# Kernel optimization log

Hardware: AMD Instinct MI355X
Metric: run time of the kernel (lower is better)

Reference implementation:

```python
import jax, jax.numpy as jnp
import numpy as np

SHAPE_ = 32          # sqrt(max_seq_len); seq positions form a SHAPE_ x SHAPE_ grid
N_HEADS = 8
BATCH = 8
SEQ_LEN = SHAPE_ * SHAPE_  # 1024
HEAD_DIM = 64


def _construct_bias(w_, s):
    """bias[..., j, i] = w_rolled[..., s - i - 1 + j]  -> (1, h, s, s).
    'full' base type: roll last axis left by one (concat of w[...,1:] and w[...,0])."""
    w_ = jnp.concatenate([w_[..., 1:], w_[..., :1]], axis=-1)  # (1, h, 2s-1)
    j = jnp.arange(s)
    i = jnp.arange(s)
    idx = (s - 1 - i)[None, :] + j[:, None]  # (s_j, s_i), values in [0, 2s-2]
    return w_[..., idx]  # (1, h, s, s), axes (..., j, i)


def setup_inputs() -> dict:
    key = jax.random.key(0)
    k1, k2 = jax.random.split(key)
    v = jax.random.normal(k1, (BATCH, SEQ_LEN, N_HEADS, HEAD_DIM), dtype=jnp.float32)
    # learned 1D bias base, length 2*SHAPE_-1 for 'full' base type
    w = jax.random.normal(k2, (1, N_HEADS, 2 * SHAPE_ - 1), dtype=jnp.float32)
    return {"v": v, "w": w}


def reference(v, w):
    s = SHAPE_
    b, L, h, d = v.shape
    bias = _construct_bias(w, s)  # (1, h, s, s)
    # x_ = bias[:, :, None, :, None, :], y_ = bias[:, :, :, None, :, None]
    # w2[., h, a, b, c, e] = bias[., h, b, e] + bias[., h, a, c]  -> (1, h, s, s, s, s)
    w2 = bias[:, :, None, :, None, :] + bias[:, :, :, None, :, None]
    w2 = w2.reshape(1, h, s * s, s * s)  # (1, h, L, L)
    # original: repeat w2 over batch then einsum('nlhd,nhlj->njhd', v, transpose(w2, [0,1,3,2]))
    # => pbv[n, j, h, d] = sum_l v[n, l, h, d] * w2[0, h, j, l]; broadcast instead of repeat.
    return jnp.einsum('nlhd,hjl->njhd', v, w2[0])
```

## Files before the change

### kernel.cpp

```cpp
#include <hip/hip_runtime.h>
#include <hip/hip_bf16.h>


#define S 32
#define HD4 128

__global__ __launch_bounds__(128) void reduce_kernel(
    const float4* __restrict__ v, float4* __restrict__ Vc,
    float4* __restrict__ Ve) {
  int block = blockIdx.x;
  int t = threadIdx.x;
  bool isVc = block < 256;
  int b2 = isVc ? block : block - 256;
  int n = b2 >> 5;
  int x = b2 & 31;
  const float4* base = v + (size_t)n * 1024 * HD4 + t;
  float4 acc = make_float4(0.f, 0.f, 0.f, 0.f);
  if (isVc) {
#pragma unroll
    for (int c = 0; c < 32; ++c) {
      float4 r = base[(size_t)(c * S + x) * HD4];
      acc.x += r.x; acc.y += r.y; acc.z += r.z; acc.w += r.w;
    }
    Vc[(size_t)b2 * HD4 + t] = acc;
  } else {
#pragma unroll
    for (int e = 0; e < 32; ++e) {
      float4 r = base[(size_t)(x * S + e) * HD4];
      acc.x += r.x; acc.y += r.y; acc.z += r.z; acc.w += r.w;
    }
    Ve[(size_t)b2 * HD4 + t] = acc;
  }
}

__global__ __launch_bounds__(256) void terms_kernel(
    const float* __restrict__ w,
    const float* __restrict__ Vc, const float* __restrict__ Ve,
    float* __restrict__ T1, float* __restrict__ T2) {
  __shared__ float bias_s[32][32];
  __shared__ float vc_s[32][64];
  __shared__ float ve_s[32][64];
  int nh = blockIdx.x;
  int n = nh >> 3, h = nh & 7;
  int t = threadIdx.x;

  for (int idx = t; idx < 1024; idx += 256) {
    int b = idx >> 5, e = idx & 31;
    int k = (32 + b - e) % 63;
    bias_s[b][e] = w[h * 63 + k];
  }
  for (int idx = t; idx < 512; idx += 256) {
    int e = idx >> 4, d4 = idx & 15;
    size_t g = ((size_t)(n * S + e) * 8 + h) * 16 + d4;
    float4 a = ((const float4*)Vc)[g];
    float4 b = ((const float4*)Ve)[g];
    vc_s[e][d4 * 4 + 0] = a.x; vc_s[e][d4 * 4 + 1] = a.y;
    vc_s[e][d4 * 4 + 2] = a.z; vc_s[e][d4 * 4 + 3] = a.w;
    ve_s[e][d4 * 4 + 0] = b.x; ve_s[e][d4 * 4 + 1] = b.y;
    ve_s[e][d4 * 4 + 2] = b.z; ve_s[e][d4 * 4 + 3] = b.w;
  }
  __syncthreads();

  int d = t & 63;
  int bg = t >> 6;
  for (int b = bg; b < 32; b += 4) {
    float a1 = 0.f, a2 = 0.f;
#pragma unroll
    for (int e = 0; e < 32; ++e) {
      a1 += bias_s[b][e] * vc_s[e][d];
      a2 += bias_s[b][e] * ve_s[e][d];
    }
    size_t g = (size_t)(n * S + b) * 512 + h * 64 + d;
    T1[g] = a1;
    T2[g] = a2;
  }
}

__global__ __launch_bounds__(256) void out_kernel(
    const float4* __restrict__ T1, const float4* __restrict__ T2,
    float4* __restrict__ out) {
  int idx = blockIdx.x * 256 + threadIdx.x;
  int d4 = idx & 15;
  int h  = (idx >> 4) & 7;
  int j  = (idx >> 7) & 1023;
  int n  = idx >> 17;
  int b = j & 31, a = j >> 5;
  float4 x = T1[((n * S + b) * 8 + h) * 16 + d4];
  float4 y = T2[((n * S + a) * 8 + h) * 16 + d4];
  out[idx] = make_float4(x.x + y.x, x.y + y.y, x.z + y.z, x.w + y.w);
}

extern "C" void kernel_launch(void* const* d_in, const int* in_sizes, int n_in,
                              void* d_out, int out_size, void* d_ws, size_t ws_size,
                              hipStream_t stream) {
  const float* v = (const float*)d_in[0];
  const float* w = (const float*)d_in[1];
  float* out = (float*)d_out;
  float* ws  = (float*)d_ws;

  float* Vc = ws;
  float* Ve = ws + 131072;
  float* T1 = ws + 262144;
  float* T2 = ws + 393216;

  reduce_kernel<<<512, 128, 0, stream>>>((const float4*)v, (float4*)Vc,
                                         (float4*)Ve);
  terms_kernel<<<64, 256, 0, stream>>>(w, Vc, Ve, T1, T2);
  out_kernel<<<4096, 256, 0, stream>>>((const float4*)T1, (const float4*)T2,
                                       (float4*)out);
}
```

Baseline: 79.18 us.

## Fuse bias-term GEMV and output broadcast into one kernel per (n,h,a)

Merges the terms kernel and the output-broadcast kernel into one kernel with 2048 blocks, each owning one (n, h, a) output slab. Each block recomputes the T1 terms for all b in shared memory plus one T2 row, then writes the 32x64 output tile directly. This removes a kernel launch and the T1/T2 global round trip, and uses more blocks than the old 64-block terms kernel. In exchange, each block redundantly recomputes the full 32x32x64 T1 product, a 32-fold duplication across the a dimension.

Measured after the change: 79.99 us. Within noise of the previous version (+1.0%).

```diff
diff --git a/kernel.cpp b/kernel.cpp
--- a/kernel.cpp
+++ b/kernel.cpp
@@ -33,61 +33,68 @@
   }
 }
 
-__global__ __launch_bounds__(256) void terms_kernel(
+__global__ __launch_bounds__(256) void fused_out_kernel(
     const float* __restrict__ w,
     const float* __restrict__ Vc, const float* __restrict__ Ve,
-    float* __restrict__ T1, float* __restrict__ T2) {
+    float4* __restrict__ out) {
   __shared__ float bias_s[32][32];
+  __shared__ float biasa_s[32];
   __shared__ float vc_s[32][64];
   __shared__ float ve_s[32][64];
-  int nh = blockIdx.x;
-  int n = nh >> 3, h = nh & 7;
-  int t = threadIdx.x;
+  __shared__ float t1_s[32][64];
+  __shared__ float t2_s[64];
+
+  int blk = blockIdx.x;
+  int a  = blk & 31;
+  int h  = (blk >> 5) & 7;
+  int n  = blk >> 8;
+  int t  = threadIdx.x;
 
   for (int idx = t; idx < 1024; idx += 256) {
     int b = idx >> 5, e = idx & 31;
-    int k = (32 + b - e) % 63;
-    bias_s[b][e] = w[h * 63 + k];
+    bias_s[b][e] = w[h * 63 + (32 + b - e) % 63];
   }
+  if (t < 32) biasa_s[t] = w[h * 63 + (32 + a - t) % 63];
+
   for (int idx = t; idx < 512; idx += 256) {
     int e = idx >> 4, d4 = idx & 15;
     size_t g = ((size_t)(n * S + e) * 8 + h) * 16 + d4;
-    float4 a = ((const float4*)Vc)[g];
-    float4 b = ((const float4*)Ve)[g];
-    vc_s[e][d4 * 4 + 0] = a.x; vc_s[e][d4 * 4 + 1] = a.y;
-    vc_s[e][d4 * 4 + 2] = a.z; vc_s[e][d4 * 4 + 3] = a.w;
-    ve_s[e][d4 * 4 + 0] = b.x; ve_s[e][d4 * 4 + 1] = b.y;
-    ve_s[e][d4 * 4 + 2] = b.z; ve_s[e][d4 * 4 + 3] = b.w;
+    float4 va = ((const float4*)Vc)[g];
+    float4 vb = ((const float4*)Ve)[g];
+    vc_s[e][d4 * 4 + 0] = va.x; vc_s[e][d4 * 4 + 1] = va.y;
+    vc_s[e][d4 * 4 + 2] = va.z; vc_s[e][d4 * 4 + 3] = va.w;
+    ve_s[e][d4 * 4 + 0] = vb.x; ve_s[e][d4 * 4 + 1] = vb.y;
+    ve_s[e][d4 * 4 + 2] = vb.z; ve_s[e][d4 * 4 + 3] = vb.w;
   }
   __syncthreads();
 
-  int d = t & 63;
+  int d  = t & 63;
   int bg = t >> 6;
+  if (t < 64) {
+    float a2 = 0.f;
+#pragma unroll
+    for (int c = 0; c < 32; ++c) a2 += biasa_s[c] * ve_s[c][t];
+    t2_s[t] = a2;
+  }
   for (int b = bg; b < 32; b += 4) {
-    float a1 = 0.f, a2 = 0.f;
+    float a1 = 0.f;
 #pragma unroll
-    for (int e = 0; e < 32; ++e) {
-      a1 += bias_s[b][e] * vc_s[e][d];
-      a2 += bias_s[b][e] * ve_s[e][d];
-    }
-    size_t g = (size_t)(n * S + b) * 512 + h * 64 + d;
-    T1[g] = a1;
-    T2[g] = a2;
+    for (int e = 0; e < 32; ++e) a1 += bias_s[b][e] * vc_s[e][d];
+    t1_s[b][d] = a1;
   }
-}
+  __syncthreads();
 
-__global__ __launch_bounds__(256) void out_kernel(
-    const float4* __restrict__ T1, const float4* __restrict__ T2,
-    float4* __restrict__ out) {
-  int idx = blockIdx.x * 256 + threadIdx.x;
-  int d4 = idx & 15;
-  int h  = (idx >> 4) & 7;
-  int j  = (idx >> 7) & 1023;
-  int n  = idx >> 17;
-  int b = j & 31, a = j >> 5;
-  float4 x = T1[((n * S + b) * 8 + h) * 16 + d4];
-  float4 y = T2[((n * S + a) * 8 + h) * 16 + d4];
-  out[idx] = make_float4(x.x + y.x, x.y + y.y, x.z + y.z, x.w + y.w);
+  const float4* t1v = (const float4*)t1_s;
+  const float4* t2v = (const float4*)t2_s;
+  size_t obase = ((size_t)(n * 1024 + a * 32) * 8 + h) * 16;
+#pragma unroll
+  for (int idx = t; idx < 512; idx += 256) {
+    int b = idx >> 4, d4 = idx & 15;
+    float4 x = t1v[b * 16 + d4];
+    float4 y = t2v[d4];
+    out[obase + (size_t)b * 128 + d4] =
+        make_float4(x.x + y.x, x.y + y.y, x.z + y.z, x.w + y.w);
+  }
 }
 
 extern "C" void kernel_launch(void* const* d_in, const int* in_sizes, int n_in,
@@ -100,12 +107,8 @@
 
   float* Vc = ws;
   float* Ve = ws + 131072;
-  float* T1 = ws + 262144;
-  float* T2 = ws + 393216;
 
   reduce_kernel<<<512, 128, 0, stream>>>((const float4*)v, (float4*)Vc,
                                          (float4*)Ve);
-  terms_kernel<<<64, 256, 0, stream>>>(w, Vc, Ve, T1, T2);
-  out_kernel<<<4096, 256, 0, stream>>>((const float4*)T1, (const float4*)T2,
-                                       (float4*)out);
+  fused_out_kernel<<<2048, 256, 0, stream>>>(w, Vc, Ve, (float4*)out);
 }
```
